# Kernel tuning notes

Hardware: AMD Instinct MI355X
Metric: run time of the kernel (lower is better)

Reference implementation:

```python
import jax, jax.numpy as jnp
import numpy as np

B, C_IN, C_OUT, H, W, K = 8, 64, 64, 128, 128, 3
KK = K * K


def _conv(x, w, b):
    # 3x3, stride 1, padding 1 (matches nn.Conv2d(stride=1, padding=1))
    y = jax.lax.conv_general_dilated(
        x, w, window_strides=(1, 1), padding=((1, 1), (1, 1)),
        dimension_numbers=('NCHW', 'OIHW', 'NCHW'))
    return y + b[None, :, None, None]


def setup_inputs() -> dict:
    key = jax.random.key(0)
    k1, k2, k3, k4, k5 = jax.random.split(key, 5)
    x = jax.random.normal(k1, (B, C_IN, H, W), jnp.float32)
    s = 1.0 / np.sqrt(C_IN * K * K)  # torch conv default init range
    w_off = jax.random.uniform(k2, (2 * KK, C_IN, K, K), jnp.float32, -s, s)
    b_off = jax.random.uniform(k3, (2 * KK,), jnp.float32, -s, s)
    w_reg = jax.random.uniform(k4, (C_OUT, C_IN, K, K), jnp.float32, -s, s)
    b_reg = jax.random.uniform(k5, (C_OUT,), jnp.float32, -s, s)
    return {"x": x, "w_off": w_off, "b_off": b_off, "w_reg": w_reg, "b_reg": b_reg}


def _deform_sample(x, offsets):
    # Equivalent of the K*K grid_sample(align_corners=True, padding_mode='zeros')
    # loop + sum over kernel positions. The norm/unnorm cancel, so sampling is
    # at absolute pixel coords base_grid + offsets.
    B_, C, H_, W_ = x.shape
    off = offsets.reshape(B_, KK, 2, H_, W_).transpose(0, 3, 4, 1, 2)  # B,H,W,KK,2
    xs = off[..., 0] + jnp.arange(W_, dtype=x.dtype)[None, None, :, None]
    ys = off[..., 1] + jnp.arange(H_, dtype=x.dtype)[None, :, None, None]
    x0 = jnp.floor(xs)
    y0 = jnp.floor(ys)
    wx1 = xs - x0
    wx0 = 1.0 - wx1
    wy1 = ys - y0
    wy0 = 1.0 - wy1
    x_flat = x.reshape(B_, C, H_ * W_)

    def gather(yi, xi, w):
        valid = (xi >= 0) & (xi < W_) & (yi >= 0) & (yi < H_)  # zeros padding
        xi_c = jnp.clip(xi, 0, W_ - 1).astype(jnp.int32)
        yi_c = jnp.clip(yi, 0, H_ - 1).astype(jnp.int32)
        idx = (yi_c * W_ + xi_c).reshape(B_, 1, H_ * W_ * KK)
        g = jnp.take_along_axis(
            x_flat, jnp.broadcast_to(idx, (B_, C, H_ * W_ * KK)), axis=2)
        g = g.reshape(B_, C, H_, W_, KK)
        wm = (w * valid.astype(x.dtype))[:, None]  # B,1,H,W,KK
        return (g * wm).sum(-1)  # sum over the KK kernel positions

    return (gather(y0, x0, wy0 * wx0)
            + gather(y0, x0 + 1.0, wy0 * wx1)
            + gather(y0 + 1.0, x0, wy1 * wx0)
            + gather(y0 + 1.0, x0 + 1.0, wy1 * wx1))


def reference(x, w_off, b_off, w_reg, b_reg):
    offsets = _conv(x, w_off, b_off)          # B, 2*KK, H, W
    sampled = _deform_sample(x, offsets)      # B, C, H, W (summed over KK)
    return _conv(sampled, w_reg, b_reg)       # B, C_OUT, H, W
```

## Files before the change

kernel.cpp:

```cpp
#include <hip/hip_runtime.h>

#define B_ 8
#define CIN 64
#define COUT 64
#define H_ 128
#define W_ 128
#define HW (H_*W_)
#define OFFP 24

typedef __attribute__((ext_vector_type(8))) short short8;
typedef __attribute__((ext_vector_type(4))) float f32x4;

__device__ __forceinline__ short f2bf(float f) {
    unsigned u = __float_as_uint(f);
    unsigned r = (u + 0x7fffu + ((u >> 16) & 1u)) >> 16;
    return (short)r;
}
__device__ __forceinline__ float bf2f(short s) {
    return __uint_as_float(((unsigned)(unsigned short)s) << 16);
}

template<int NT>
__device__ __forceinline__ void prep_one(const float* __restrict__ w, short* __restrict__ o,
                                         int i, int n_used) {
    int j = i & 7, lane = (i >> 3) & 63, rest = i >> 9;
    int nt = rest % NT, dc = rest / NT, c = dc & 1, d = dc >> 1;
    int oc = nt * 16 + (lane & 15);
    int ic = c * 32 + (lane >> 4) * 8 + j;
    float v = (oc < n_used) ? w[(oc * 64 + ic) * 9 + d] : 0.f;
    o[i] = f2bf(v);
}

__global__ __launch_bounds__(256) void k_tr(const float* __restrict__ x,
                                            short* __restrict__ xt,
                                            const float* __restrict__ wof,
                                            const float* __restrict__ wrg,
                                            short* __restrict__ wt1,
                                            short* __restrict__ wt2) {
    int i = blockIdx.x * 256 + threadIdx.x;
    if (i < 9 * 2 * 2 * 512) prep_one<2>(wof, wt1, i, 18);
    if (i < 9 * 2 * 4 * 512) prep_one<4>(wrg, wt2, i, 64);

    __shared__ float tile[64 * 129];
    int bh = blockIdx.x;
    int bb = bh & 7, h = bh >> 3;
    const float* xp = x + (size_t)bb * (CIN * HW) + h * W_;
#pragma unroll
    for (int j = 0; j < 32; ++j) {
        int e = threadIdx.x + 256 * j;
        int cc = e >> 7, ww = e & 127;
        tile[cc * 129 + ww] = __builtin_nontemporal_load(xp + cc * HW + ww);
    }
    __syncthreads();
    short* op = xt + (((size_t)(bb << 7) + h) << 13);
#pragma unroll
    for (int j = 0; j < 4; ++j) {
        int t = threadIdx.x + 256 * j;
        int ww = t >> 3, c0 = (t & 7) << 3;
        short8 o;
#pragma unroll
        for (int k = 0; k < 8; ++k) o[k] = f2bf(tile[(c0 + k) * 129 + ww]);
        *(short8*)(op + ww * 64 + c0) = o;
    }
}

__device__ __forceinline__ void prep3(const unsigned* __restrict__ myo, int g,
                                      int w, int h, int cko,
                                      int* __restrict__ eo, float* __restrict__ wg) {
#pragma unroll
    for (int t = 0; t < 3; ++t) {
        unsigned owk = myo[g * 3 + t];
        float ox = bf2f((short)(owk & 0xffff));
        float oy = bf2f((short)(owk >> 16));
        float xs = (float)w + ox, ys = (float)h + oy;
        float x0f = floorf(xs), y0f = floorf(ys);
        float wx1 = xs - x0f, wx0 = 1.f - wx1;
        float wy1 = ys - y0f, wy0 = 1.f - wy1;
        int x0 = (int)x0f, y0 = (int)y0f;
        int x1 = x0 + 1, y1 = y0 + 1;
        int x0c = min(max(x0, 0), W_ - 1), x1c = min(max(x1, 0), W_ - 1);
        int y0c = min(max(y0, 0), H_ - 1), y1c = min(max(y1, 0), H_ - 1);
        bool vx0 = ((unsigned)x0 < W_), vx1 = ((unsigned)x1 < W_);
        bool vy0 = ((unsigned)y0 < H_), vy1 = ((unsigned)y1 < H_);
        wg[t * 4 + 0] = (vy0 && vx0) ? wy0 * wx0 : 0.f;
        wg[t * 4 + 1] = (vy0 && vx1) ? wy0 * wx1 : 0.f;
        wg[t * 4 + 2] = (vy1 && vx0) ? wy1 * wx0 : 0.f;
        wg[t * 4 + 3] = (vy1 && vx1) ? wy1 * wx1 : 0.f;
        eo[t * 4 + 0] = ((y0c * W_ + x0c) << 6) + cko;
        eo[t * 4 + 1] = ((y0c * W_ + x1c) << 6) + cko;
        eo[t * 4 + 2] = ((y1c * W_ + x0c) << 6) + cko;
        eo[t * 4 + 3] = ((y1c * W_ + x1c) << 6) + cko;
    }
}

__global__ __launch_bounds__(512, 4) void k_c1s(const short* __restrict__ xt,
                                                const short* __restrict__ wt1,
                                                const float* __restrict__ bof,
                                                short* __restrict__ smp) {
    __shared__ short lds[33280 + 6144];
    short* A = lds;
    unsigned short* St = (unsigned short*)(lds + 33280);
    int blk = blockIdx.x, tid = threadIdx.x;
    int bb = blk & 7;
    int h0 = (blk >> 3) << 1;

#pragma unroll
    for (int it = 0; it < 9; ++it) {
        int s = tid + it * 512;
        if (s < 4160) {
            int r = s / 1040, rem = s % 1040;
            int px = rem >> 3, ck = rem & 7;
            int y = h0 - 1 + r, xx = px - 1;
            bool v = ((unsigned)y < H_) && ((unsigned)xx < W_);
            int yc = min(max(y, 0), H_ - 1), xc = min(max(xx, 0), W_ - 1);
            short8 val = *(const short8*)(xt + ((((size_t)(bb << 7) + yc) << 7) + xc) * 64 + ck * 8);
            short8 z = {0, 0, 0, 0, 0, 0, 0, 0};
            if (!v) val = z;
            *(short8*)(&A[(r * 130 + px) * 64 + ((ck ^ (px & 7)) << 3)]) = val;
        }
    }
    __syncthreads();

    int lane = tid & 63;
    int wave = tid >> 6;
    int lr = wave >> 2;
    int p0 = (wave & 3) * 32;
    int m = lane & 15, quad = lane >> 4;

    {
        f32x4 acc[2][2];
#pragma unroll
        for (int nt = 0; nt < 2; ++nt) {
            int oc = nt * 16 + m;
            float bv = (oc < 18) ? bof[oc] : 0.f;
#pragma unroll
            for (int mt = 0; mt < 2; ++mt) {
                acc[mt][nt][0] = bv; acc[mt][nt][1] = bv;
                acc[mt][nt][2] = bv; acc[mt][nt][3] = bv;
            }
        }
#pragma unroll
        for (int d = 0; d < 9; ++d) {
            int dy = d / 3, dx = d % 3;
#pragma unroll
            for (int c = 0; c < 2; ++c) {
                short8 a[2];
#pragma unroll
                for (int mt = 0; mt < 2; ++mt) {
                    int px = p0 + mt * 16 + m + dx;
                    a[mt] = *(const short8*)(&A[((lr + dy) * 130 + px) * 64 + (((c * 4 + quad) ^ (px & 7)) << 3)]);
                }
#pragma unroll
                for (int nt = 0; nt < 2; ++nt) {
                    short8 b = *(const short8*)(wt1 + ((((d * 2 + c) * 2 + nt) * 64 + lane) << 3));
#pragma unroll
                    for (int mt = 0; mt < 2; ++mt)
                        acc[mt][nt] = __builtin_amdgcn_mfma_f32_16x16x32_bf16(a[mt], b, acc[mt][nt], 0, 0, 0);
                }
            }
        }
#pragma unroll
        for (int nt = 0; nt < 2; ++nt) {
            int oc = nt * 16 + m;
            if (oc < 18) {
#pragma unroll
                for (int mt = 0; mt < 2; ++mt) {
                    int pl = lr * 128 + p0 + mt * 16 + quad * 4;
#pragma unroll
                    for (int r = 0; r < 4; ++r)
                        St[(pl + r) * OFFP + oc] = (unsigned short)f2bf(acc[mt][nt][r]);
                }
            }
        }
    }
    __syncthreads();

    {
        int ck = tid & 7, sxb = tid >> 3;
        int cko = ck * 8;
        const short* xim = xt + ((size_t)bb << 20);
#pragma unroll
        for (int row = 0; row < 2; ++row) {
            int y = h0 + row;
#pragma unroll
            for (int hf = 0; hf < 2; ++hf) {
                int sx = sxb + hf * 64;
                const unsigned* myo = (const unsigned*)(St + (row * 128 + sx) * OFFP);
                float acc[8];
#pragma unroll
                for (int i = 0; i < 8; ++i) acc[i] = 0.f;
#pragma unroll
                for (int g = 0; g < 3; ++g) {
                    int eo[12]; float wg[12]; short8 v[12];
                    prep3(myo, g, sx, y, cko, eo, wg);
#pragma unroll
                    for (int n = 0; n < 12; ++n) v[n] = *(const short8*)(xim + eo[n]);
#pragma unroll
                    for (int n = 0; n < 12; ++n) {
                        float wv = wg[n];
#pragma unroll
                        for (int i = 0; i < 8; ++i) acc[i] += wv * bf2f(v[n][i]);
                    }
                }
                short8 o;
#pragma unroll
                for (int i = 0; i < 8; ++i) o[i] = f2bf(acc[i]);
                *(short8*)(smp + ((((size_t)(bb << 7) + y) << 7) + sx) * 64 + cko) = o;
            }
        }
    }
}

__global__ __launch_bounds__(512, 4) void k_conv2(const short* __restrict__ smp,
                                                  const short* __restrict__ wt2,
                                                  const float* __restrict__ brg,
                                                  float* __restrict__ out) {
    __shared__ short A[4 * 130 * 64];
    int blk = blockIdx.x, tid = threadIdx.x;
    int bb = blk & 7;
    int h0 = (blk >> 3) << 1;

#pragma unroll
    for (int it = 0; it < 9; ++it) {
        int s = tid + it * 512;
        if (s < 4160) {
            int r = s / 1040, rem = s % 1040;
            int px = rem >> 3, ck = rem & 7;
            int y = h0 - 1 + r, xx = px - 1;
            bool v = ((unsigned)y < H_) && ((unsigned)xx < W_);
            int yc = min(max(y, 0), H_ - 1), xc = min(max(xx, 0), W_ - 1);
            short8 val = *(const short8*)(smp + ((((size_t)(bb << 7) + yc) << 7) + xc) * 64 + ck * 8);
            short8 z = {0, 0, 0, 0, 0, 0, 0, 0};
            if (!v) val = z;
            *(short8*)(&A[(r * 130 + px) * 64 + ((ck ^ (px & 7)) << 3)]) = val;
        }
    }
    __syncthreads();

    int lane = tid & 63;
    int wave = tid >> 6;
    int lr = wave >> 2;
    int p0 = (wave & 3) * 32;
    int m = lane & 15, quad = lane >> 4;

    f32x4 acc[2][4];
#pragma unroll
    for (int nt = 0; nt < 4; ++nt) {
        float bv = brg[nt * 16 + m];
#pragma unroll
        for (int mt = 0; mt < 2; ++mt) {
            acc[mt][nt][0] = bv; acc[mt][nt][1] = bv;
            acc[mt][nt][2] = bv; acc[mt][nt][3] = bv;
        }
    }
#pragma unroll
    for (int d = 0; d < 9; ++d) {
        int dy = d / 3, dx = d % 3;
#pragma unroll
        for (int c = 0; c < 2; ++c) {
            short8 a[2];
#pragma unroll
            for (int mt = 0; mt < 2; ++mt) {
                int px = p0 + mt * 16 + m + dx;
                a[mt] = *(const short8*)(&A[((lr + dy) * 130 + px) * 64 + (((c * 4 + quad) ^ (px & 7)) << 3)]);
            }
#pragma unroll
            for (int nt = 0; nt < 4; ++nt) {
                short8 b = *(const short8*)(wt2 + ((((d * 2 + c) * 4 + nt) * 64 + lane) << 3));
#pragma unroll
                for (int mt = 0; mt < 2; ++mt)
                    acc[mt][nt] = __builtin_amdgcn_mfma_f32_16x16x32_bf16(a[mt], b, acc[mt][nt], 0, 0, 0);
            }
        }
    }
#pragma unroll
    for (int nt = 0; nt < 4; ++nt) {
        int oc = nt * 16 + m;
#pragma unroll
        for (int mt = 0; mt < 2; ++mt) {
            int wpix = p0 + mt * 16 + quad * 4;
            __builtin_nontemporal_store(acc[mt][nt],
                (f32x4*)(out + (((size_t)(bb * 64 + oc)) << 14) + ((h0 + lr) << 7) + wpix));
        }
    }
}

extern "C" void kernel_launch(void* const* d_in, const int* in_sizes, int n_in,
                              void* d_out, int out_size, void* d_ws, size_t ws_size,
                              hipStream_t stream) {
    const float* x   = (const float*)d_in[0];
    const float* wof = (const float*)d_in[1];
    const float* bof = (const float*)d_in[2];
    const float* wrg = (const float*)d_in[3];
    const float* brg = (const float*)d_in[4];
    float* out = (float*)d_out;

    char* ws = (char*)d_ws;
    short* xt  = (short*)ws;
    short* smp = (short*)(ws + 16777216);
    short* wt1 = (short*)(ws + 2 * 16777216);
    short* wt2 = (short*)(ws + 2 * 16777216 + 36864);

    k_tr   <<<dim3(B_ * H_),     256, 0, stream>>>(x, xt, wof, wrg, wt1, wt2);
    k_c1s  <<<dim3(B_ * H_ / 2), 512, 0, stream>>>(xt, wt1, bof, smp);
    k_conv2<<<dim3(B_ * H_ / 2), 512, 0, stream>>>(smp, wt2, brg, out);
}
```

Before: 147.3 us.

## Stage conv tiles via direct global-to-LDS loads and precompute bilinear taps in LDS

```diff
diff --git a/kernel.cpp b/kernel.cpp
--- a/kernel.cpp
+++ b/kernel.cpp
@@ -9,6 +9,7 @@
 #define OFFP 24
 
 typedef __attribute__((ext_vector_type(8))) short short8;
+typedef __attribute__((ext_vector_type(4))) short s16x4;
 typedef __attribute__((ext_vector_type(4))) float f32x4;
 
 __device__ __forceinline__ short f2bf(float f) {
@@ -64,61 +65,84 @@
     }
 }
 
-__device__ __forceinline__ void prep3(const unsigned* __restrict__ myo, int g,
-                                      int w, int h, int cko,
-                                      int* __restrict__ eo, float* __restrict__ wg) {
-#pragma unroll
-    for (int t = 0; t < 3; ++t) {
-        unsigned owk = myo[g * 3 + t];
-        float ox = bf2f((short)(owk & 0xffff));
-        float oy = bf2f((short)(owk >> 16));
-        float xs = (float)w + ox, ys = (float)h + oy;
-        float x0f = floorf(xs), y0f = floorf(ys);
-        float wx1 = xs - x0f, wx0 = 1.f - wx1;
-        float wy1 = ys - y0f, wy0 = 1.f - wy1;
-        int x0 = (int)x0f, y0 = (int)y0f;
-        int x1 = x0 + 1, y1 = y0 + 1;
-        int x0c = min(max(x0, 0), W_ - 1), x1c = min(max(x1, 0), W_ - 1);
-        int y0c = min(max(y0, 0), H_ - 1), y1c = min(max(y1, 0), H_ - 1);
-        bool vx0 = ((unsigned)x0 < W_), vx1 = ((unsigned)x1 < W_);
-        bool vy0 = ((unsigned)y0 < H_), vy1 = ((unsigned)y1 < H_);
-        wg[t * 4 + 0] = (vy0 && vx0) ? wy0 * wx0 : 0.f;
-        wg[t * 4 + 1] = (vy0 && vx1) ? wy0 * wx1 : 0.f;
-        wg[t * 4 + 2] = (vy1 && vx0) ? wy1 * wx0 : 0.f;
-        wg[t * 4 + 3] = (vy1 && vx1) ? wy1 * wx1 : 0.f;
-        eo[t * 4 + 0] = ((y0c * W_ + x0c) << 6) + cko;
-        eo[t * 4 + 1] = ((y0c * W_ + x1c) << 6) + cko;
-        eo[t * 4 + 2] = ((y1c * W_ + x0c) << 6) + cko;
-        eo[t * 4 + 3] = ((y1c * W_ + x1c) << 6) + cko;
-    }
+__device__ __forceinline__ void stage4(short* A, const short* __restrict__ src,
+                                       int bb, int h0, int tid) {
+    int wv = tid >> 6, l = tid & 63;
+    int r = wv >> 1, half = wv & 1;
+    int y = h0 - 1 + r;
+    int P0 = 1 + half * 64;
+    int px0 = P0 + (l >> 3);
+    int ckl = l & 7;
+    if ((unsigned)y < H_) {
+        int ckg = ckl ^ (px0 & 7);
+        const short* gp = src + ((((size_t)(bb << 7) + y) << 7) + (px0 - 1)) * 64 + ckg * 8;
+#pragma unroll
+        for (int i = 0; i < 8; ++i) {
+            short* lp = &A[(r * 130 + P0 + i * 8) * 64];
+            __builtin_amdgcn_global_load_lds(
+                (const __attribute__((address_space(1))) void*)(gp + i * 512),
+                (__attribute__((address_space(3))) void*)lp, 16, 0, 0);
+        }
+    } else {
+        short8 z = {0, 0, 0, 0, 0, 0, 0, 0};
+#pragma unroll
+        for (int i = 0; i < 8; ++i)
+            *(short8*)(&A[(r * 130 + P0 + i * 8) * 64 + l * 8]) = z;
+    }
+    if (tid < 64) {
+        int rr = tid >> 4, side = (tid >> 3) & 1, ck = tid & 7;
+        int px = side * 129;
+        short8 z = {0, 0, 0, 0, 0, 0, 0, 0};
+        *(short8*)(&A[(rr * 130 + px) * 64 + ((ck ^ (px & 7)) << 3)]) = z;
+    }
+}
+
+__device__ __forceinline__ void prep_task(int t, int h0,
+                                          const unsigned short* __restrict__ St,
+                                          s16x4* __restrict__ idxs,
+                                          f32x4* __restrict__ wgs) {
+    int pxl = (int)((unsigned)t / 9u);
+    int tap = t - pxl * 9;
+    int row = pxl >> 7, sx = pxl & 127;
+    unsigned owk = *(const unsigned*)(St + pxl * OFFP + tap * 2);
+    float ox = bf2f((short)(owk & 0xffff));
+    float oy = bf2f((short)(owk >> 16));
+    float xs = (float)sx + ox, ys = (float)(h0 + row) + oy;
+    float x0f = floorf(xs), y0f = floorf(ys);
+    float wx1 = xs - x0f, wx0 = 1.f - wx1;
+    float wy1 = ys - y0f, wy0 = 1.f - wy1;
+    int x0 = (int)x0f, y0 = (int)y0f;
+    int x1 = x0 + 1, y1 = y0 + 1;
+    int x0c = min(max(x0, 0), W_ - 1), x1c = min(max(x1, 0), W_ - 1);
+    int y0c = min(max(y0, 0), H_ - 1), y1c = min(max(y1, 0), H_ - 1);
+    bool vx0 = ((unsigned)x0 < W_), vx1 = ((unsigned)x1 < W_);
+    bool vy0 = ((unsigned)y0 < H_), vy1 = ((unsigned)y1 < H_);
+    f32x4 wg;
+    wg[0] = (vy0 && vx0) ? wy0 * wx0 : 0.f;
+    wg[1] = (vy0 && vx1) ? wy0 * wx1 : 0.f;
+    wg[2] = (vy1 && vx0) ? wy1 * wx0 : 0.f;
+    wg[3] = (vy1 && vx1) ? wy1 * wx1 : 0.f;
+    s16x4 id;
+    id[0] = (short)(y0c * W_ + x0c);
+    id[1] = (short)(y0c * W_ + x1c);
+    id[2] = (short)(y1c * W_ + x0c);
+    id[3] = (short)(y1c * W_ + x1c);
+    idxs[t] = id;
+    wgs[t] = wg;
 }
 
 __global__ __launch_bounds__(512, 4) void k_c1s(const short* __restrict__ xt,
                                                 const short* __restrict__ wt1,
                                                 const float* __restrict__ bof,
                                                 short* __restrict__ smp) {
-    __shared__ short lds[33280 + 6144];
+    __shared__ __align__(16) short lds[33280 + 6144];
     short* A = lds;
     unsigned short* St = (unsigned short*)(lds + 33280);
     int blk = blockIdx.x, tid = threadIdx.x;
     int bb = blk & 7;
     int h0 = (blk >> 3) << 1;
 
-#pragma unroll
-    for (int it = 0; it < 9; ++it) {
-        int s = tid + it * 512;
-        if (s < 4160) {
-            int r = s / 1040, rem = s % 1040;
-            int px = rem >> 3, ck = rem & 7;
-            int y = h0 - 1 + r, xx = px - 1;
-            bool v = ((unsigned)y < H_) && ((unsigned)xx < W_);
-            int yc = min(max(y, 0), H_ - 1), xc = min(max(xx, 0), W_ - 1);
-            short8 val = *(const short8*)(xt + ((((size_t)(bb << 7) + yc) << 7) + xc) * 64 + ck * 8);
-            short8 z = {0, 0, 0, 0, 0, 0, 0, 0};
-            if (!v) val = z;
-            *(short8*)(&A[(r * 130 + px) * 64 + ((ck ^ (px & 7)) << 3)]) = val;
-        }
-    }
+    stage4(A, xt, bb, h0, tid);
     __syncthreads();
 
     int lane = tid & 63;
@@ -175,6 +199,15 @@
     }
     __syncthreads();
 
+    s16x4* idxs = (s16x4*)lds;
+    f32x4*  wgs  = (f32x4*)(lds + 9216);
+    {
+#pragma unroll
+        for (int k = 0; k < 4; ++k) prep_task(tid + 512 * k, h0, St, idxs, wgs);
+        if (tid < 256) prep_task(2048 + tid, h0, St, idxs, wgs);
+    }
+    __syncthreads();
+
     {
         int ck = tid & 7, sxb = tid >> 3;
         int cko = ck * 8;
@@ -185,21 +218,30 @@
 #pragma unroll
             for (int hf = 0; hf < 2; ++hf) {
                 int sx = sxb + hf * 64;
-                const unsigned* myo = (const unsigned*)(St + (row * 128 + sx) * OFFP);
+                int pb = (row * 128 + sx) * 9;
                 float acc[8];
 #pragma unroll
                 for (int i = 0; i < 8; ++i) acc[i] = 0.f;
 #pragma unroll
                 for (int g = 0; g < 3; ++g) {
-                    int eo[12]; float wg[12]; short8 v[12];
-                    prep3(myo, g, sx, y, cko, eo, wg);
+                    int eo[12]; float wf[12]; short8 v[12];
+#pragma unroll
+                    for (int t2 = 0; t2 < 3; ++t2) {
+                        s16x4 id = idxs[pb + g * 3 + t2];
+                        f32x4 wv = wgs[pb + g * 3 + t2];
+#pragma unroll
+                        for (int c = 0; c < 4; ++c) {
+                            eo[t2 * 4 + c] = (((int)id[c]) << 6) + cko;
+                            wf[t2 * 4 + c] = wv[c];
+                        }
+                    }
 #pragma unroll
                     for (int n = 0; n < 12; ++n) v[n] = *(const short8*)(xim + eo[n]);
 #pragma unroll
                     for (int n = 0; n < 12; ++n) {
-                        float wv = wg[n];
-#pragma unroll
-                        for (int i = 0; i < 8; ++i) acc[i] += wv * bf2f(v[n][i]);
+                        float wvv = wf[n];
+#pragma unroll
+                        for (int i = 0; i < 8; ++i) acc[i] += wvv * bf2f(v[n][i]);
                     }
                 }
                 short8 o;
@@ -215,26 +257,12 @@
                                                   const short* __restrict__ wt2,
                                                   const float* __restrict__ brg,
                                                   float* __restrict__ out) {
-    __shared__ short A[4 * 130 * 64];
+    __shared__ __align__(16) short A[4 * 130 * 64];
     int blk = blockIdx.x, tid = threadIdx.x;
     int bb = blk & 7;
     int h0 = (blk >> 3) << 1;
 
-#pragma unroll
-    for (int it = 0; it < 9; ++it) {
-        int s = tid + it * 512;
-        if (s < 4160) {
-            int r = s / 1040, rem = s % 1040;
-            int px = rem >> 3, ck = rem & 7;
-            int y = h0 - 1 + r, xx = px - 1;
-            bool v = ((unsigned)y < H_) && ((unsigned)xx < W_);
-            int yc = min(max(y, 0), H_ - 1), xc = min(max(xx, 0), W_ - 1);
-            short8 val = *(const short8*)(smp + ((((size_t)(bb << 7) + yc) << 7) + xc) * 64 + ck * 8);
-            short8 z = {0, 0, 0, 0, 0, 0, 0, 0};
-            if (!v) val = z;
-            *(short8*)(&A[(r * 130 + px) * 64 + ((ck ^ (px & 7)) << 3)]) = val;
-        }
-    }
+    stage4(A, smp, bb, h0, tid);
     __syncthreads();
 
     int lane = tid & 63;
```

Result: faster. 143.4 us (-2.6%).
